# Performance work log

Measured on AMD Instinct MI355X. Metric: run time of the kernel, lower is better.

The kernel has to match this reference:

```python
import jax, jax.numpy as jnp
import numpy as np

NUM_BINS = 23
SIGMA_RATIO = 0.5
SMOOTH_NR = 1e-07
SMOOTH_DR = 1e-07

BIN_CENTERS = jnp.linspace(0.0, 1.0, NUM_BINS)  # [bins]
_sigma = jnp.mean(BIN_CENTERS[1:] - BIN_CENTERS[:-1]) * SIGMA_RATIO
PRETERM = 1.0 / (2.0 * _sigma ** 2)


def setup_inputs() -> dict:
    key = jax.random.key(0)
    k1, k2 = jax.random.split(key)
    shape = (4, 1, 96, 96, 96)
    pred = jax.random.uniform(k1, shape, dtype=jnp.float32)
    target = jax.random.uniform(k2, shape, dtype=jnp.float32)
    return {"pred": pred, "target": target}


def _parzen(img):
    # img: [B, ...] -> weight [B, N, bins], probability [B, 1, bins]
    img = jnp.clip(img, 0.0, 1.0)
    img = img.reshape(img.shape[0], -1, 1)  # [B, N, 1]
    weight = jnp.exp(-PRETERM * (img - BIN_CENTERS[None, None, :]) ** 2)  # [B, N, bins]
    weight = weight / jnp.sum(weight, axis=-1, keepdims=True)
    probability = jnp.mean(weight, axis=-2, keepdims=True)  # [B, 1, bins]
    return weight, probability


def reference(pred, target):
    wa, pa = _parzen(pred)    # wa: [B, N, bins]
    wb, pb = _parzen(target)
    n = wa.shape[1]
    # joint histogram: [B, bins, bins]
    pab = jnp.einsum('bni,bnj->bij', wa, wb) / n
    # marginal product: [B, bins, bins]
    papb = jnp.einsum('bki,bkj->bij', pa, pb)
    mi = jnp.sum(pab * jnp.log((pab + SMOOTH_NR) / (papb + SMOOTH_DR) + SMOOTH_DR), axis=(1, 2))
    return -jnp.mean(mi)
```

## Files before the change

### kernel.cpp

```cpp
#include <hip/hip_runtime.h>
#include <math.h>


#define NBINS   23
#define NCELLS  529
#define NBATCH  4
#define NVOX    884736
#define PBLK    432
#define RS      72
#define IMGB    (32 * RS * 2)
#define WREG    (2 * IMGB)

typedef float    vf4  __attribute__((ext_vector_type(4)));
typedef _Float16 h8   __attribute__((ext_vector_type(8)));
typedef float    f16v __attribute__((ext_vector_type(16)));

#define G1 0.13533528f
#define G2 3.3546263e-4f
#define G3 1.5229979e-8f

__device__ __forceinline__ float window7(float x, int& i0, float* w)
{
    x = fminf(fmaxf(x, 0.0f), 1.0f);
    int ka = (int)floorf(fmaf(x, 22.0f, 0.5f));
    i0 = min(max(ka - 3, 0), 16);
    float v  = fmaf((float)(i0 + 3), -(1.0f / 22.0f), x);
    float W0 = __expf(-968.0f * v * v);
    float R  = __expf(88.0f * v);
    float Ri = __builtin_amdgcn_rcpf(R);
    float R2 = R * R,   R3 = R2 * R;
    float R2i = Ri * Ri, R3i = R2i * Ri;
    w[0] = W0 * (R3i * G3);
    w[1] = W0 * (R2i * G2);
    w[2] = W0 * (Ri  * G1);
    w[3] = W0;
    w[4] = W0 * (R   * G1);
    w[5] = W0 * (R2  * G2);
    w[6] = W0 * (R3  * G3);
    return ((w[0] + w[6]) + (w[1] + w[5])) + ((w[2] + w[4]) + w[3]);
}

__global__ __launch_bounds__(256)
void mi_mfma(const float* __restrict__ pred,
             const float* __restrict__ targ,
             float* __restrict__ partial)
{
    __shared__ __align__(16) char smem[4 * WREG];

    const int p    = blockIdx.x;
    const int b    = blockIdx.y;
    const int wv   = threadIdx.x >> 6;
    const int lane = threadIdx.x & 63;
    const int m    = lane & 31;
    const int h    = lane >> 5;

    char* wbase = smem + wv * WREG;
    _Float16* Aimg = (_Float16*)wbase;
    _Float16* Bimg = (_Float16*)(wbase + IMGB);

    const size_t base = (size_t)b * NVOX + (size_t)p * 2048 + (size_t)wv * 512
                      + (size_t)lane * 8;
    const vf4* __restrict__ px4 = (const vf4*)(pred + base);
    const vf4* __restrict__ py4 = (const vf4*)(targ + base);
    vf4 xa = px4[0], xb = px4[1], ya = py4[0], yb = py4[1];
    float xs[8] = {xa.x, xa.y, xa.z, xa.w, xb.x, xb.y, xb.z, xb.w};
    float ys[8] = {ya.x, ya.y, ya.z, ya.w, yb.x, yb.y, yb.z, yb.w};

    f16v acc = {};

    #pragma unroll
    for (int c = 0; c < 8; ++c) {
        vf4 z = {0.f, 0.f, 0.f, 0.f};
        #pragma unroll
        for (int it = 0; it < 4; ++it) {
            *(vf4*)(wbase        + (it * 64 + lane) * 16) = z;
            *(vf4*)(wbase + IMGB + (it * 64 + lane) * 16) = z;
        }

        int ia, ja;
        float wa[7], wb[7];
        float sa = window7(xs[c], ia, wa);
        float sb = window7(ys[c], ja, wb);
        float inv = __builtin_amdgcn_rcpf(sa * sb);

        #pragma unroll
        for (int t = 0; t < 7; ++t) {
            Aimg[(ia + t) * RS + lane] = (_Float16)(wa[t] * inv);
            Bimg[(ja + t) * RS + lane] = (_Float16)wb[t];
        }

        #pragma unroll
        for (int s = 0; s < 4; ++s) {
            h8 Af = *(const h8*)(Aimg + m * RS + 16 * s + 8 * h);
            h8 Bf = *(const h8*)(Bimg + m * RS + 16 * s + 8 * h);
            acc = __builtin_amdgcn_mfma_f32_32x32x16_f16(Af, Bf, acc, 0, 0, 0);
        }
    }

    float* tile = (float*)wbase;
    #pragma unroll
    for (int r = 0; r < 16; ++r) {
        int row = (r & 3) + 8 * (r >> 2) + 4 * h;
        tile[row * 33 + m] = acc[r];
    }
    __syncthreads();
    for (int c = threadIdx.x; c < NCELLS; c += 256) {
        int i = c / NBINS, j = c % NBINS;
        float s = 0.0f;
        #pragma unroll
        for (int w = 0; w < 4; ++w)
            s += ((const float*)(smem + w * WREG))[i * 33 + j];
        partial[((size_t)(b * PBLK + p)) * NCELLS + c] = s;
    }
}

__global__ __launch_bounds__(64)
void mi_reduce(const float* __restrict__ partial, double* __restrict__ pab64)
{
    const int c = blockIdx.x, b = blockIdx.y;
    double s = 0.0;
    for (int t = threadIdx.x; t < PBLK; t += 64)
        s += (double)partial[((size_t)(b * PBLK + t)) * NCELLS + c];
    #pragma unroll
    for (int off = 32; off > 0; off >>= 1) s += __shfl_down(s, off, 64);
    if (threadIdx.x == 0) pab64[b * NCELLS + c] = s * (1.0 / (double)NVOX);
}

__global__ __launch_bounds__(256)
void mi_final(const double* __restrict__ pab64, float* __restrict__ out)
{
    __shared__ double s_pab[NCELLS];
    __shared__ double s_pa[NBINS];
    __shared__ double s_pb[NBINS];
    __shared__ double s_red[4];

    double total = 0.0;
    for (int b = 0; b < NBATCH; ++b) {
        for (int c = threadIdx.x; c < NCELLS; c += 256)
            s_pab[c] = pab64[b * NCELLS + c];
        __syncthreads();
        if (threadIdx.x < NBINS) {
            const int i = threadIdx.x;
            double r = 0.0, cl = 0.0;
            for (int j = 0; j < NBINS; ++j) {
                r  += s_pab[i * NBINS + j];
                cl += s_pab[j * NBINS + i];
            }
            s_pa[i] = r; s_pb[i] = cl;
        }
        __syncthreads();
        double t = 0.0;
        for (int c = threadIdx.x; c < NCELLS; c += 256) {
            double pv   = s_pab[c];
            double papb = s_pa[c / NBINS] * s_pb[c % NBINS];
            t += pv * log((pv + 1e-7) / (papb + 1e-7) + 1e-7);
        }
        #pragma unroll
        for (int off = 32; off > 0; off >>= 1) t += __shfl_down(t, off, 64);
        if ((threadIdx.x & 63) == 0) s_red[threadIdx.x >> 6] = t;
        __syncthreads();
        if (threadIdx.x == 0) total += s_red[0] + s_red[1] + s_red[2] + s_red[3];
        __syncthreads();
    }
    if (threadIdx.x == 0) out[0] = (float)(-total * 0.25);
}

extern "C" void kernel_launch(void* const* d_in, const int* in_sizes, int n_in,
                              void* d_out, int out_size, void* d_ws, size_t ws_size,
                              hipStream_t stream)
{
    const float* pred = (const float*)d_in[0];
    const float* targ = (const float*)d_in[1];
    float* out = (float*)d_out;
    char* ws = (char*)d_ws;

    const size_t off_partial = 0;
    const size_t off_pab64   =
        ((size_t)NBATCH * PBLK * NCELLS * 4 + 255) & ~(size_t)255;

    float*  partial = (float*)(ws + off_partial);
    double* pab64   = (double*)(ws + off_pab64);

    mi_mfma  <<<dim3(PBLK,   NBATCH), 256, 0, stream>>>(pred, targ, partial);
    mi_reduce<<<dim3(NCELLS, NBATCH),  64, 0, stream>>>(partial, pab64);
    mi_final <<<1, 256, 0, stream>>>(pab64, out);
}
```

Before: 109.2 us.

## Fuse partial reduction and MI finalization into one per-batch kernel

Replaces the separate reduce kernel (529x4 blocks of 64 threads) and the single-block final kernel with one kernel of 4 blocks, one per batch. Each block sums all partial tiles for its batch and computes that batch's MI term, then adds it to the output with an atomic, which needs a memset first. The zeroing loop in the MFMA kernel also now clears only the rows the tile reads. This cuts launches and the intermediate pab buffer, but leaves just 4 blocks to stream roughly 3.6 MB of partials, which limits parallelism in the reduction.

```diff
diff --git a/kernel.cpp b/kernel.cpp
--- a/kernel.cpp
+++ b/kernel.cpp
@@ -72,9 +72,13 @@
     for (int c = 0; c < 8; ++c) {
         vf4 z = {0.f, 0.f, 0.f, 0.f};
         #pragma unroll
-        for (int it = 0; it < 4; ++it) {
+        for (int it = 0; it < 3; ++it) {
             *(vf4*)(wbase        + (it * 64 + lane) * 16) = z;
             *(vf4*)(wbase + IMGB + (it * 64 + lane) * 16) = z;
+        }
+        if (lane < 24) {
+            *(vf4*)(wbase        + (192 + lane) * 16) = z;
+            *(vf4*)(wbase + IMGB + (192 + lane) * 16) = z;
         }
 
         int ia, ja;
@@ -114,55 +118,56 @@
     }
 }
 
-__global__ __launch_bounds__(64)
-void mi_reduce(const float* __restrict__ partial, double* __restrict__ pab64)
+__global__ __launch_bounds__(256)
+void mi_batch(const float* __restrict__ partial, float* __restrict__ out)
 {
-    const int c = blockIdx.x, b = blockIdx.y;
-    double s = 0.0;
-    for (int t = threadIdx.x; t < PBLK; t += 64)
-        s += (double)partial[((size_t)(b * PBLK + t)) * NCELLS + c];
-    #pragma unroll
-    for (int off = 32; off > 0; off >>= 1) s += __shfl_down(s, off, 64);
-    if (threadIdx.x == 0) pab64[b * NCELLS + c] = s * (1.0 / (double)NVOX);
-}
+    const int b = blockIdx.x;
+    const int t = threadIdx.x;
+    const float* __restrict__ src = partial + (size_t)b * PBLK * NCELLS;
 
-__global__ __launch_bounds__(256)
-void mi_final(const double* __restrict__ pab64, float* __restrict__ out)
-{
+    double a0 = 0.0, a1 = 0.0, a2 = 0.0;
+    for (int p = 0; p < PBLK; ++p) {
+        const float* __restrict__ row = src + (size_t)p * NCELLS;
+        a0 += (double)row[t];
+        a1 += (double)row[256 + t];
+        if (t < NCELLS - 512) a2 += (double)row[512 + t];
+    }
+
     __shared__ double s_pab[NCELLS];
     __shared__ double s_pa[NBINS];
     __shared__ double s_pb[NBINS];
     __shared__ double s_red[4];
 
-    double total = 0.0;
-    for (int b = 0; b < NBATCH; ++b) {
-        for (int c = threadIdx.x; c < NCELLS; c += 256)
-            s_pab[c] = pab64[b * NCELLS + c];
-        __syncthreads();
-        if (threadIdx.x < NBINS) {
-            const int i = threadIdx.x;
-            double r = 0.0, cl = 0.0;
-            for (int j = 0; j < NBINS; ++j) {
-                r  += s_pab[i * NBINS + j];
-                cl += s_pab[j * NBINS + i];
-            }
-            s_pa[i] = r; s_pb[i] = cl;
+    const double invn = 1.0 / (double)NVOX;
+    s_pab[t]       = a0 * invn;
+    s_pab[256 + t] = a1 * invn;
+    if (t < NCELLS - 512) s_pab[512 + t] = a2 * invn;
+    __syncthreads();
+
+    if (t < NBINS) {
+        double r = 0.0, cl = 0.0;
+        for (int j = 0; j < NBINS; ++j) {
+            r  += s_pab[t * NBINS + j];
+            cl += s_pab[j * NBINS + t];
         }
-        __syncthreads();
-        double t = 0.0;
-        for (int c = threadIdx.x; c < NCELLS; c += 256) {
-            double pv   = s_pab[c];
-            double papb = s_pa[c / NBINS] * s_pb[c % NBINS];
-            t += pv * log((pv + 1e-7) / (papb + 1e-7) + 1e-7);
-        }
-        #pragma unroll
-        for (int off = 32; off > 0; off >>= 1) t += __shfl_down(t, off, 64);
-        if ((threadIdx.x & 63) == 0) s_red[threadIdx.x >> 6] = t;
-        __syncthreads();
-        if (threadIdx.x == 0) total += s_red[0] + s_red[1] + s_red[2] + s_red[3];
-        __syncthreads();
+        s_pa[t] = r; s_pb[t] = cl;
     }
-    if (threadIdx.x == 0) out[0] = (float)(-total * 0.25);
+    __syncthreads();
+
+    double s = 0.0;
+    for (int c = t; c < NCELLS; c += 256) {
+        double pv   = s_pab[c];
+        double papb = s_pa[c / NBINS] * s_pb[c % NBINS];
+        s += pv * log((pv + 1e-7) / (papb + 1e-7) + 1e-7);
+    }
+    #pragma unroll
+    for (int off = 32; off > 0; off >>= 1) s += __shfl_down(s, off, 64);
+    if ((t & 63) == 0) s_red[t >> 6] = s;
+    __syncthreads();
+    if (t == 0) {
+        double mi = s_red[0] + s_red[1] + s_red[2] + s_red[3];
+        atomicAdd(out, (float)(-mi * 0.25));
+    }
 }
 
 extern "C" void kernel_launch(void* const* d_in, const int* in_sizes, int n_in,
@@ -172,16 +177,9 @@
     const float* pred = (const float*)d_in[0];
     const float* targ = (const float*)d_in[1];
     float* out = (float*)d_out;
-    char* ws = (char*)d_ws;
+    float* partial = (float*)d_ws;
 
-    const size_t off_partial = 0;
-    const size_t off_pab64   =
-        ((size_t)NBATCH * PBLK * NCELLS * 4 + 255) & ~(size_t)255;
-
-    float*  partial = (float*)(ws + off_partial);
-    double* pab64   = (double*)(ws + off_pab64);
-
-    mi_mfma  <<<dim3(PBLK,   NBATCH), 256, 0, stream>>>(pred, targ, partial);
-    mi_reduce<<<dim3(NCELLS, NBATCH),  64, 0, stream>>>(partial, pab64);
-    mi_final <<<1, 256, 0, stream>>>(pab64, out);
+    (void)hipMemsetAsync(d_out, 0, sizeof(float), stream);
+    mi_mfma <<<dim3(PBLK, NBATCH), 256, 0, stream>>>(pred, targ, partial);
+    mi_batch<<<NBATCH, 256, 0, stream>>>(partial, out);
 }
```

Measured after the change: 215.4 us. 1.97x slower.
